# Optimization experiments

Hardware: AMD Instinct MI355X
Metric: run time of the kernel (lower is better)

The kernel has to match this reference:

```python
import jax, jax.numpy as jnp
import numpy as np

K_NN = 32
LN_EPS = 1e-5
P_JOINT = 0.95      # safety_priorities['structural_joints']
P_PLATFORM = 0.9    # safety_priorities['working_platforms']


def _sqdist(a, b):
    # a:[B,M,3], b:[B,N,3] -> [B,M,N] squared euclidean distances
    return jnp.maximum(jnp.sum(a * a, -1)[:, :, None] + jnp.sum(b * b, -1)[:, None, :]
                       - 2.0 * jnp.einsum('bmd,bnd->bmn', a, b), 0.0)


def _gather(arr, idx):
    # arr:[B,N,D], idx:[B,C] -> [B,C,D]
    B, C = idx.shape
    return jnp.take_along_axis(arr, jnp.broadcast_to(idx[:, :, None], (B, C, arr.shape[-1])), axis=1)


def _fps(coords, num_samples):
    # iterative farthest point sampling (deterministic start at index 0)
    B, N, _ = coords.shape
    start = jnp.zeros((B,), jnp.int32)
    dist0 = jnp.full((B, N), jnp.inf, coords.dtype)
    samp0 = jnp.zeros((B, num_samples), jnp.int32)

    def body(i, carry):
        dist, samp, last = carry
        last_pts = _gather(coords, last[:, None])                 # [B,1,3]
        d = jnp.sqrt(jnp.sum((coords - last_pts) ** 2, -1))       # [B,N]
        dist = jnp.minimum(dist, d)
        nxt = jnp.argmax(dist, 1).astype(jnp.int32)
        dist = dist.at[jnp.arange(B), nxt].set(0.0)
        samp = samp.at[:, i].set(nxt)
        return dist, samp, nxt

    _, samp, _ = jax.lax.fori_loop(1, num_samples, body, (dist0, samp0, start))
    return samp


def _safety(coords, scale):
    # per-point safety score [B,N], computed on the full point cloud (as in original)
    N = coords.shape[1]
    z = coords[:, :, 2]
    if scale == 'global':
        return 1.0 + jax.nn.sigmoid((z - z.mean(1, keepdims=True)) / 5.0) * P_JOINT
    if scale == 'component':
        zv = jnp.var(z, axis=1, keepdims=True, ddof=1)            # torch.var is unbiased
        return jnp.broadcast_to(1.0 + jnp.exp(-zv / 0.1) * P_PLATFORM, z.shape)
    # detail: full NxN cdist -> connection density (dist < 0.5  <=>  sqdist < 0.25)
    d2 = _sqdist(coords, coords)                                  # [B,N,N]
    density = jnp.sum(d2 < 0.25, -1).astype(coords.dtype)
    return 1.0 + density / N * P_JOINT


def _select_scale(features, coords, C, S, W1, b1, W2, b2, scale):
    idx = _fps(coords, C)                     # [B,C]
    cfeat = _gather(features, idx)            # [B,C,D]
    ccoord = _gather(coords, idx)             # [B,C,3]
    # kNN max-pooled local features (computed by original module; not used downstream)
    knn_d2 = _sqdist(ccoord, coords)          # [B,C,N]
    _, knn = jax.lax.top_k(-knn_d2, K_NN)
    _local = jax.vmap(lambda f, i: f[i])(features, knn).max(2)    # [B,C,D]
    # per-center safety score: per-point score gathered at FPS centers
    safety = jnp.take_along_axis(_safety(coords, scale), idx, axis=1)  # [B,C]
    # selector MLP: Linear -> ReLU -> Linear -> Sigmoid
    probs = jax.nn.sigmoid(jnp.maximum(cfeat @ W1.T + b1, 0.0) @ W2.T + b2)  # [B,C,S]
    final = probs.mean(-1) * safety           # [B,C] per-center score
    _, top = jax.lax.top_k(final, S)          # [B,S]
    return _gather(cfeat, top)                # [B,S,D]


def _forward(pf, pc, g_W1, g_b1, g_W2, g_b2, c_W1, c_b1, c_W2, c_b2,
             d_W1, d_b1, d_W2, d_b2, p_W1, p_b1, p_W2, p_b2, ln_g, ln_b):
    g = _select_scale(pf, pc, 256, 16, g_W1, g_b1, g_W2, g_b2, 'global')
    c = _select_scale(pf, pc, 128, 16, c_W1, c_b1, c_W2, c_b2, 'component')
    d = _select_scale(pf, pc, 64, 8, d_W1, d_b1, d_W2, d_b2, 'detail')
    toks = jnp.concatenate([g, c, d], 1)      # [B,40,D]
    # prompt_mlp: Linear(D,D/2) -> ReLU -> Linear(D/2,D) -> LayerNorm(D)
    h = jnp.maximum(toks @ p_W1.T + p_b1, 0.0) @ p_W2.T + p_b2
    mu = h.mean(-1, keepdims=True)
    var = h.var(-1, keepdims=True)
    return (h - mu) * jax.lax.rsqrt(var + LN_EPS) * ln_g + ln_b


def setup_inputs() -> dict:
    key = jax.random.key(0)
    B, N, D = 2, 8192, 768
    ks = iter(jax.random.split(key, 32))

    def nrm(shape, s=0.02):
        return jax.random.normal(next(ks), shape, jnp.float32) * s

    inp = {
        'point_features': jax.random.normal(next(ks), (B, N, D), jnp.float32),
        'point_coords': jax.random.normal(next(ks), (B, N, 3), jnp.float32) * 2.0,
    }
    for p, C, S in [('g', 256, 16), ('c', 128, 16), ('d', 64, 8)]:
        inp[p + '_W1'] = nrm((C, D)); inp[p + '_b1'] = jnp.zeros((C,), jnp.float32)
        inp[p + '_W2'] = nrm((S, C)); inp[p + '_b2'] = jnp.zeros((S,), jnp.float32)
    inp['p_W1'] = nrm((D // 2, D)); inp['p_b1'] = jnp.zeros((D // 2,), jnp.float32)
    inp['p_W2'] = nrm((D, D // 2)); inp['p_b2'] = jnp.zeros((D,), jnp.float32)
    inp['ln_g'] = jnp.ones((D,), jnp.float32); inp['ln_b'] = jnp.zeros((D,), jnp.float32)
    return inp


def reference(point_features, point_coords, g_W1, g_b1, g_W2, g_b2,
              c_W1, c_b1, c_W2, c_b2, d_W1, d_b1, d_W2, d_b2,
              p_W1, p_b1, p_W2, p_b2, ln_g, ln_b):
    return _forward(point_features, point_coords, g_W1, g_b1, g_W2, g_b2,
                    c_W1, c_b1, c_W2, c_b2, d_W1, d_b1, d_W2, d_b2,
                    p_W1, p_b1, p_W2, p_b2, ln_g, ln_b)
```

## Files before the change

### kernel.cpp

```cpp
#include <hip/hip_runtime.h>
#include <math.h>

#define N_PTS 8192
#define D_FEAT 768

typedef float v2f __attribute__((ext_vector_type(2)));

__device__ __forceinline__ float wred_max_f32(float x) {
    int v = __float_as_int(x), o;
    o = __builtin_amdgcn_update_dpp(0, v, 0x111, 0xf, 0xf, false); v = __float_as_int(fmaxf(__int_as_float(v), __int_as_float(o)));
    o = __builtin_amdgcn_update_dpp(0, v, 0x112, 0xf, 0xf, false); v = __float_as_int(fmaxf(__int_as_float(v), __int_as_float(o)));
    o = __builtin_amdgcn_update_dpp(0, v, 0x114, 0xf, 0xf, false); v = __float_as_int(fmaxf(__int_as_float(v), __int_as_float(o)));
    o = __builtin_amdgcn_update_dpp(0, v, 0x118, 0xf, 0xf, false); v = __float_as_int(fmaxf(__int_as_float(v), __int_as_float(o)));
    o = __builtin_amdgcn_update_dpp(0, v, 0x142, 0xa, 0xf, false); v = __float_as_int(fmaxf(__int_as_float(v), __int_as_float(o)));
    o = __builtin_amdgcn_update_dpp(0, v, 0x143, 0xc, 0xf, false); v = __float_as_int(fmaxf(__int_as_float(v), __int_as_float(o)));
    return __int_as_float(__builtin_amdgcn_readlane(v, 63));
}
__device__ __forceinline__ int wred_min_i32(int x) {
    int v = x, o;
    o = __builtin_amdgcn_update_dpp(0x7fffffff, v, 0x111, 0xf, 0xf, false); v = (o < v) ? o : v;
    o = __builtin_amdgcn_update_dpp(0x7fffffff, v, 0x112, 0xf, 0xf, false); v = (o < v) ? o : v;
    o = __builtin_amdgcn_update_dpp(0x7fffffff, v, 0x114, 0xf, 0xf, false); v = (o < v) ? o : v;
    o = __builtin_amdgcn_update_dpp(0x7fffffff, v, 0x118, 0xf, 0xf, false); v = (o < v) ? o : v;
    o = __builtin_amdgcn_update_dpp(0x7fffffff, v, 0x142, 0xa, 0xf, false); v = (o < v) ? o : v;
    o = __builtin_amdgcn_update_dpp(0x7fffffff, v, 0x143, 0xc, 0xf, false); v = (o < v) ? o : v;
    return __builtin_amdgcn_readlane(v, 63);
}
__device__ __forceinline__ float wred_add_f32(float x) {
    int v = __float_as_int(x), o;
    o = __builtin_amdgcn_update_dpp(0, v, 0x111, 0xf, 0xf, false); v = __float_as_int(__int_as_float(v) + __int_as_float(o));
    o = __builtin_amdgcn_update_dpp(0, v, 0x112, 0xf, 0xf, false); v = __float_as_int(__int_as_float(v) + __int_as_float(o));
    o = __builtin_amdgcn_update_dpp(0, v, 0x114, 0xf, 0xf, false); v = __float_as_int(__int_as_float(v) + __int_as_float(o));
    o = __builtin_amdgcn_update_dpp(0, v, 0x118, 0xf, 0xf, false); v = __float_as_int(__int_as_float(v) + __int_as_float(o));
    o = __builtin_amdgcn_update_dpp(0, v, 0x142, 0xa, 0xf, false); v = __float_as_int(__int_as_float(v) + __int_as_float(o));
    o = __builtin_amdgcn_update_dpp(0, v, 0x143, 0xc, 0xf, false); v = __float_as_int(__int_as_float(v) + __int_as_float(o));
    return __int_as_float(__builtin_amdgcn_readlane(v, 63));
}

#define DPP64_STEP(cur, ctrl, rmask)                                                        \
    {                                                                                       \
        unsigned _h = (unsigned)__builtin_amdgcn_update_dpp(0, (int)(unsigned)((cur) >> 32), ctrl, rmask, 0xf, false); \
        unsigned _l = (unsigned)__builtin_amdgcn_update_dpp(0, (int)(unsigned)(cur), ctrl, rmask, 0xf, false);         \
        unsigned long long _o = ((unsigned long long)_h << 32) | _l;                        \
        cur = (_o > (cur)) ? _o : (cur);                                                    \
    }

__global__ __launch_bounds__(512, 2) __attribute__((amdgpu_waves_per_eu(2)))
void fps_kernel(const float* __restrict__ coords,
                int* __restrict__ idx_all,
                float* __restrict__ safety_all) {
#pragma clang fp contract(off)
    const int b = blockIdx.x;
    const int t = threadIdx.x;
    const float* cb = coords + (size_t)b * N_PTS * 3;

    v2f px2[8], py2[8], pz2[8], m2p[8];
#pragma unroll
    for (int j = 0; j < 8; j++) {
        int p0 = t + (2 * j) * 512, p1 = t + (2 * j + 1) * 512;
        px2[j].x = cb[p0 * 3 + 0]; px2[j].y = cb[p1 * 3 + 0];
        py2[j].x = cb[p0 * 3 + 1]; py2[j].y = cb[p1 * 3 + 1];
        pz2[j].x = cb[p0 * 3 + 2]; pz2[j].y = cb[p1 * 3 + 2];
        m2p[j].x = INFINITY; m2p[j].y = INFINITY;
    }
    __shared__ float cbl4[N_PTS * 4];
    __shared__ unsigned long long skey[2][8];
    __shared__ int sel[256];
    __shared__ float r1s[8], r2s[8];
#pragma unroll
    for (int j = 0; j < 8; j++) {
        int p0 = t + (2 * j) * 512, p1 = t + (2 * j + 1) * 512;
        *(float4*)&cbl4[p0 * 4] = make_float4(px2[j].x, py2[j].x, pz2[j].x, 0.f);
        *(float4*)&cbl4[p1 * 4] = make_float4(px2[j].y, py2[j].y, pz2[j].y, 0.f);
    }
    if (t == 0) sel[0] = 0;
    float lx = cb[0], ly = cb[1], lz = cb[2];
    __syncthreads();

    const int lane = t & 63, w = t >> 6;
    for (int i = 1; i < 256; i++) {
        v2f Lx = {lx, lx}, Ly = {ly, ly}, Lz = {lz, lz};
#pragma unroll
        for (int j = 0; j < 8; j++) {
            v2f dx = px2[j] - Lx, dy = py2[j] - Ly, dz = pz2[j] - Lz;
            v2f d2 = dx * dx + dy * dy + dz * dz;
            m2p[j] = __builtin_elementwise_min(m2p[j], d2);
        }
        v2f q[4];
#pragma unroll
        for (int j = 0; j < 4; j++) q[j] = __builtin_elementwise_max(m2p[j], m2p[j + 4]);
        q[0] = __builtin_elementwise_max(q[0], q[2]);
        q[1] = __builtin_elementwise_max(q[1], q[3]);
        q[0] = __builtin_elementwise_max(q[0], q[1]);
        float c2 = fmaxf(q[0].x, q[0].y);
        int ci[8];
#pragma unroll
        for (int j = 0; j < 8; j++) {
            int a  = (m2p[j].x == c2) ? (2 * j)     : 0x7fff;
            int bb = (m2p[j].y == c2) ? (2 * j + 1) : 0x7fff;
            ci[j] = (a < bb) ? a : bb;
        }
#pragma unroll
        for (int j = 0; j < 4; j++) ci[j] = min(ci[j], ci[j + 4]);
        int bk = min(min(ci[0], ci[1]), min(ci[2], ci[3]));
        float thi = c2 * 0.9999995f;
        int tot = 0;
#pragma unroll
        for (int j = 0; j < 8; j++) {
            tot += __popcll(__ballot(m2p[j].x >= thi));
            tot += __popcll(__ballot(m2p[j].y >= thi));
        }
        float smax;
        if (tot > 64) {
            smax = -1.f; bk = 0;
#pragma unroll
            for (int k = 0; k < 16; k++) {
                float mk = (k & 1) ? m2p[k >> 1].y : m2p[k >> 1].x;
                float s = sqrtf(mk);
                if (s > smax) { smax = s; bk = k; }
            }
        } else {
            smax = sqrtf(c2);
        }
        int bi = t + bk * 512;
        unsigned long long key = ((unsigned long long)__float_as_uint(smax) << 32)
                               | (unsigned)(0xFFFFFFFFu - (unsigned)bi);
        DPP64_STEP(key, 0x111, 0xf)
        DPP64_STEP(key, 0x112, 0xf)
        DPP64_STEP(key, 0x114, 0xf)
        DPP64_STEP(key, 0x118, 0xf)
        DPP64_STEP(key, 0x142, 0xa)
        DPP64_STEP(key, 0x143, 0xc)
        if (lane == 63) skey[i & 1][w] = key;
        __syncthreads();
        const int par = i & 1;
        unsigned long long k8 = skey[par][lane & 7];
        int cidx = (int)(0xFFFFFFFFu - (unsigned)k8);
        float spec = 0.f;
        if (lane < 24) spec = cbl4[cidx * 4 + (lane >> 3)];
        DPP64_STEP(k8, 0x111, 0xf)
        DPP64_STEP(k8, 0x112, 0xf)
        DPP64_STEP(k8, 0x114, 0xf)
        unsigned klo = (unsigned)__builtin_amdgcn_readlane((int)(unsigned)k8, 7);
        int fbi = (int)(0xFFFFFFFFu - klo);
        int ww = (fbi & 511) >> 6;
        lx = __int_as_float(__builtin_amdgcn_readlane(__float_as_int(spec), ww));
        ly = __int_as_float(__builtin_amdgcn_readlane(__float_as_int(spec), 8 + ww));
        lz = __int_as_float(__builtin_amdgcn_readlane(__float_as_int(spec), 16 + ww));
        if (t == 0) sel[i] = fbi;
    }

    __syncthreads();
    if (t < 256) {
        int v = sel[t];
        idx_all[b * 256 + t] = v;
        if (t < 128) idx_all[512 + b * 128 + t] = v;
        if (t < 64)  idx_all[768 + b * 64 + t] = v;
    }

    float s1 = 0.f, s2 = 0.f;
#pragma unroll
    for (int j = 0; j < 8; j++) {
        s1 += pz2[j].x; s2 += pz2[j].x * pz2[j].x;
        s1 += pz2[j].y; s2 += pz2[j].y * pz2[j].y;
    }
    s1 = wred_add_f32(s1);
    s2 = wred_add_f32(s2);
    if (lane == 0) { r1s[w] = s1; r2s[w] = s2; }
    __syncthreads();
    float S1 = ((r1s[0] + r1s[1]) + (r1s[2] + r1s[3])) + ((r1s[4] + r1s[5]) + (r1s[6] + r1s[7]));
    float S2 = ((r2s[0] + r2s[1]) + (r2s[2] + r2s[3])) + ((r2s[4] + r2s[5]) + (r2s[6] + r2s[7]));
    float mean = S1 / 8192.0f;
    float var1 = (S2 - S1 * S1 / 8192.0f) / 8191.0f;
    float scomp = 1.0f + expf(-var1 / 0.1f) * 0.9f;
    if (t < 256) {
        int p = sel[t];
        float z = cbl4[p * 4 + 2];
        safety_all[b * 256 + t] = 1.0f + (1.0f / (1.0f + expf(-((z - mean) / 5.0f)))) * 0.95f;
        if (t < 128) safety_all[512 + b * 128 + t] = scomp;
    }
}

__global__ __launch_bounds__(256) void score_kernel(
    const float* __restrict__ feat, const float* __restrict__ coords,
    const float* __restrict__ gW1, const float* __restrict__ gb1,
    const float* __restrict__ gW2, const float* __restrict__ gb2,
    const float* __restrict__ cW1, const float* __restrict__ cb1,
    const float* __restrict__ cW2, const float* __restrict__ cb2,
    const float* __restrict__ dW1, const float* __restrict__ db1,
    const float* __restrict__ dW2, const float* __restrict__ db2,
    const int* __restrict__ idx_all, const float* __restrict__ safety_all,
    float* __restrict__ final_all) {
    int bid = blockIdx.x;
    int b, c0, C, S, off;
    const float *W1, *b1, *W2, *b2;
    if (bid < 64)      { C = 256; S = 16; W1 = gW1; b1 = gb1; W2 = gW2; b2 = gb2; b = bid >> 5; c0 = (bid & 31) * 8; off = 0; }
    else if (bid < 96) { int r = bid - 64; C = 128; S = 16; W1 = cW1; b1 = cb1; W2 = cW2; b2 = cb2; b = r >> 4; c0 = (r & 15) * 8; off = 512; }
    else               { int r = bid - 96; C = 64;  S = 8;  W1 = dW1; b1 = db1; W2 = dW2; b2 = db2; b = r >> 3; c0 = (r & 7) * 8; off = 768; }
    const bool isdet = (bid >= 96);

    __shared__ float xt[8 * 772];
    __shared__ float h1s[8 * 260];
    __shared__ float ps[8 * 16];
    __shared__ int pid[8];
    __shared__ float dpart[4][8];
    __shared__ float sdens[8];
    const int t = threadIdx.x;
    if (t < 8) pid[t] = idx_all[off + b * C + c0 + t];
    __syncthreads();

    if (isdet) {
#pragma clang fp contract(off)
        float cx[8], cy[8], cz[8], cc[8];
#pragma unroll
        for (int c = 0; c < 8; c++) {
            const float* cp = coords + ((size_t)b * N_PTS + pid[c]) * 3;
            cx[c] = cp[0]; cy[c] = cp[1]; cz[c] = cp[2];
            cc[c] = cx[c] * cx[c] + cy[c] * cy[c] + cz[c] * cz[c];
        }
        int cnt[8];
#pragma unroll
        for (int c = 0; c < 8; c++) cnt[c] = 0;
        const float* cbl = coords + (size_t)b * N_PTS * 3;
        for (int k = 0; k < 32; k++) {
            int q = t + k * 256;
            float x = cbl[q * 3], y = cbl[q * 3 + 1], z = cbl[q * 3 + 2];
            float pp = x * x + y * y + z * z;
#pragma unroll
            for (int c = 0; c < 8; c++) {
                float dot = cx[c] * x + cy[c] * y + cz[c] * z;
                float d2 = (cc[c] + pp) - 2.0f * dot;
                if (d2 < 0.25f) cnt[c]++;
            }
        }
        int wv = t >> 6;
#pragma unroll
        for (int c = 0; c < 8; c++) {
            float s = wred_add_f32((float)cnt[c]);
            if ((t & 63) == 0) dpart[wv][c] = s;
        }
    }

    for (int r = 0; r < 8; r++) {
        const float* src = feat + ((size_t)b * N_PTS + pid[r]) * D_FEAT;
        for (int c = t; c < 768; c += 256) xt[r * 772 + c] = src[c];
    }
    __syncthreads();
    if (isdet && t < 8) {
        float tot = dpart[0][t] + dpart[1][t] + dpart[2][t] + dpart[3][t];
        sdens[t] = 1.0f + (tot / 8192.0f) * 0.95f;
    }

    {
        int rp = t & 3;
        int jg = t >> 2;
        int r0 = rp * 2;
        if (jg * 4 < C) {
            float4 acc0[4], acc1[4];
#pragma unroll
            for (int a = 0; a < 4; a++) { acc0[a] = make_float4(0, 0, 0, 0); acc1[a] = make_float4(0, 0, 0, 0); }
            for (int k = 0; k < 768; k += 4) {
                float4 x0 = *(const float4*)&xt[r0 * 772 + k];
                float4 x1 = *(const float4*)&xt[(r0 + 1) * 772 + k];
#pragma unroll
                for (int a = 0; a < 4; a++) {
                    int j = jg * 4 + a;
                    float4 wv = *(const float4*)&W1[(size_t)j * 768 + k];
                    acc0[a].x = fmaf(wv.x, x0.x, acc0[a].x); acc0[a].y = fmaf(wv.y, x0.y, acc0[a].y);
                    acc0[a].z = fmaf(wv.z, x0.z, acc0[a].z); acc0[a].w = fmaf(wv.w, x0.w, acc0[a].w);
                    acc1[a].x = fmaf(wv.x, x1.x, acc1[a].x); acc1[a].y = fmaf(wv.y, x1.y, acc1[a].y);
                    acc1[a].z = fmaf(wv.z, x1.z, acc1[a].z); acc1[a].w = fmaf(wv.w, x1.w, acc1[a].w);
                }
            }
#pragma unroll
            for (int a = 0; a < 4; a++) {
                int j = jg * 4 + a;
                float bb = b1[j];
                float v0 = (acc0[a].x + acc0[a].y) + (acc0[a].z + acc0[a].w) + bb;
                float v1 = (acc1[a].x + acc1[a].y) + (acc1[a].z + acc1[a].w) + bb;
                h1s[r0 * 260 + j]       = fmaxf(v0, 0.f);
                h1s[(r0 + 1) * 260 + j] = fmaxf(v1, 0.f);
            }
        }
    }
    __syncthreads();

    if (t < 8 * S) {
        int r = t / S, s = t % S;
        float4 a = make_float4(0, 0, 0, 0);
        for (int k = 0; k < C; k += 4) {
            float4 wv = *(const float4*)&W2[s * C + k];
            float4 h = *(const float4*)&h1s[r * 260 + k];
            a.x = fmaf(wv.x, h.x, a.x); a.y = fmaf(wv.y, h.y, a.y);
            a.z = fmaf(wv.z, h.z, a.z); a.w = fmaf(wv.w, h.w, a.w);
        }
        float logit = (a.x + a.y) + (a.z + a.w) + b2[s];
        ps[r * 16 + s] = 1.0f / (1.0f + expf(-logit));
    }
    __syncthreads();
    if (t < 8) {
        float m = 0.f;
        for (int s = 0; s < S; s++) m += ps[t * 16 + s];
        m /= (float)S;
        float saf = isdet ? sdens[t] : safety_all[off + b * C + c0 + t];
        final_all[off + b * C + c0 + t] = m * saf;
    }
}

__global__ __launch_bounds__(256) void final_kernel(
    const float* __restrict__ feat, const int* __restrict__ idx_all,
    const float* __restrict__ final_all,
    const float* __restrict__ pW1, const float* __restrict__ pb1,
    const float* __restrict__ pW2, const float* __restrict__ pb2,
    const float* __restrict__ lng, const float* __restrict__ lnb,
    float* __restrict__ out) {
    int bid = blockIdx.x;
    int b = bid / 20, pr = bid % 20;
    int t = threadIdx.x;
    __shared__ float xt[2 * 772];
    __shared__ float h1s[2 * 388];
    __shared__ float red[16];
    __shared__ int tokp[2];

    int scale = (pr < 8) ? 0 : (pr < 16) ? 1 : 2;
    int C    = (scale == 0) ? 256 : (scale == 1) ? 128 : 64;
    int off  = (scale == 0) ? 0 : (scale == 1) ? 512 : 768;
    int base = (scale == 0) ? 0 : (scale == 1) ? 8 : 16;
    int r0 = (pr - base) * 2;

    if (t < 64) {
        float v[4];
#pragma unroll
        for (int j = 0; j < 4; j++) {
            int ii = t + j * 64;
            v[j] = (ii < C) ? final_all[off + b * C + ii] : -INFINITY;
        }
        for (int s = 0; s <= r0 + 1; s++) {
            float bd = v[0]; int bj = 0;
#pragma unroll
            for (int j = 1; j < 4; j++) if (v[j] > bd) { bd = v[j]; bj = j; }
            int bi2 = t + bj * 64;
            float m = wred_max_f32(bd);
            int cand = (bd == m) ? bi2 : 0x7fffffff;
            int wi = wred_min_i32(cand);
            if (t == (wi & 63)) {
#pragma unroll
                for (int j = 0; j < 4; j++) if (j == (wi >> 6)) v[j] = -INFINITY;
            }
            if (t == 0) {
                if (s == r0)     tokp[0] = idx_all[off + b * C + wi];
                if (s == r0 + 1) tokp[1] = idx_all[off + b * C + wi];
            }
        }
    }
    __syncthreads();

    for (int r = 0; r < 2; r++) {
        int p = tokp[r];
        const float* src = feat + ((size_t)b * N_PTS + p) * D_FEAT;
        for (int c = t; c < 768; c += 256) xt[r * 772 + c] = src[c];
    }
    __syncthreads();

    for (int u = t; u < 768; u += 256) {
        int j = u >> 1, r = u & 1;
        float4 a = make_float4(0, 0, 0, 0);
        for (int k = 0; k < 768; k += 4) {
            float4 wv = *(const float4*)&pW1[(size_t)j * 768 + k];
            float4 x = *(const float4*)&xt[r * 772 + k];
            a.x = fmaf(wv.x, x.x, a.x); a.y = fmaf(wv.y, x.y, a.y);
            a.z = fmaf(wv.z, x.z, a.z); a.w = fmaf(wv.w, x.w, a.w);
        }
        float v = (a.x + a.y) + (a.z + a.w) + pb1[j];
        h1s[r * 388 + j] = fmaxf(v, 0.f);
    }
    __syncthreads();

    for (int u = t; u < 1536; u += 256) {
        int o = u >> 1, r = u & 1;
        float4 a = make_float4(0, 0, 0, 0);
        for (int k = 0; k < 384; k += 4) {
            float4 wv = *(const float4*)&pW2[(size_t)o * 384 + k];
            float4 h = *(const float4*)&h1s[r * 388 + k];
            a.x = fmaf(wv.x, h.x, a.x); a.y = fmaf(wv.y, h.y, a.y);
            a.z = fmaf(wv.z, h.z, a.z); a.w = fmaf(wv.w, h.w, a.w);
        }
        xt[r * 772 + o] = (a.x + a.y) + (a.z + a.w) + pb2[o];
    }
    __syncthreads();

    for (int r = 0; r < 2; r++) {
        float s1 = 0.f, s2 = 0.f;
        for (int o = t; o < 768; o += 256) { float v = xt[r * 772 + o]; s1 += v; s2 += v * v; }
#pragma unroll
        for (int off2 = 32; off2 >= 1; off2 >>= 1) {
            s1 += __shfl_down(s1, off2, 64);
            s2 += __shfl_down(s2, off2, 64);
        }
        int lane = t & 63, wid = t >> 6;
        if (lane == 0) { red[wid * 2] = s1; red[wid * 2 + 1] = s2; }
        __syncthreads();
        float S1 = red[0] + red[2] + red[4] + red[6];
        float S2 = red[1] + red[3] + red[5] + red[7];
        float mu = S1 / 768.0f;
        float var = S2 / 768.0f - mu * mu;
        float inv = rsqrtf(var + 1e-5f);
        float* dst = out + ((size_t)b * 40 + pr * 2 + r) * 768;
        for (int o = t; o < 768; o += 256) {
            float v = xt[r * 772 + o];
            dst[o] = (v - mu) * inv * lng[o] + lnb[o];
        }
        __syncthreads();
    }
}

extern "C" void kernel_launch(void* const* d_in, const int* in_sizes, int n_in,
                              void* d_out, int out_size, void* d_ws, size_t ws_size,
                              hipStream_t stream) {
    const float* feat   = (const float*)d_in[0];
    const float* coords = (const float*)d_in[1];
    const float* gW1 = (const float*)d_in[2],  *gb1 = (const float*)d_in[3];
    const float* gW2 = (const float*)d_in[4],  *gb2 = (const float*)d_in[5];
    const float* cW1 = (const float*)d_in[6],  *cb1 = (const float*)d_in[7];
    const float* cW2 = (const float*)d_in[8],  *cb2 = (const float*)d_in[9];
    const float* dW1 = (const float*)d_in[10], *db1 = (const float*)d_in[11];
    const float* dW2 = (const float*)d_in[12], *db2 = (const float*)d_in[13];
    const float* pW1 = (const float*)d_in[14], *pb1 = (const float*)d_in[15];
    const float* pW2 = (const float*)d_in[16], *pb2 = (const float*)d_in[17];
    const float* lng = (const float*)d_in[18], *lnb = (const float*)d_in[19];
    float* out = (float*)d_out;

    int*   idx_all    = (int*)d_ws;
    float* safety_all = (float*)d_ws + 896;
    float* final_all  = (float*)d_ws + 1792;

    fps_kernel<<<2, 512, 0, stream>>>(coords, idx_all, safety_all);
    score_kernel<<<112, 256, 0, stream>>>(feat, coords, gW1, gb1, gW2, gb2, cW1, cb1, cW2, cb2,
                                          dW1, db1, dW2, db2, idx_all, safety_all, final_all);
    final_kernel<<<40, 256, 0, stream>>>(feat, idx_all, final_all, pW1, pb1, pW2, pb2, lng, lnb, out);
}
```

Before: 558.0 us.

## Split final MLP into top-k, GEMM and layernorm kernels, retile score GEMM

The FPS argmax reduction now does a float max, then a ballot to find the winning lane, with an integer-min fallback on ties, in place of 64-bit DPP key reductions. The score kernel's W1 GEMM is re-tiled so each thread processes all 8 rows over a quarter of K, and the four K-partials are reduced through shared memory. The monolithic final kernel, which redundantly recomputed top-k and loaded whole weight matrices per block, is split into separate top-k, hidden-layer, output-layer and layernorm kernels spread over more blocks. This adds launches and global round-trips for intermediates.

```diff
diff --git a/kernel.cpp b/kernel.cpp
--- a/kernel.cpp
+++ b/kernel.cpp
@@ -123,14 +123,18 @@
             smax = sqrtf(c2);
         }
         int bi = t + bk * 512;
-        unsigned long long key = ((unsigned long long)__float_as_uint(smax) << 32)
-                               | (unsigned)(0xFFFFFFFFu - (unsigned)bi);
-        DPP64_STEP(key, 0x111, 0xf)
-        DPP64_STEP(key, 0x112, 0xf)
-        DPP64_STEP(key, 0x114, 0xf)
-        DPP64_STEP(key, 0x118, 0xf)
-        DPP64_STEP(key, 0x142, 0xa)
-        DPP64_STEP(key, 0x143, 0xc)
+        float mred = wred_max_f32(smax);
+        unsigned long long ball = __ballot(smax == mred);
+        int bi_win;
+        if (__popcll(ball) == 1) {
+            int ls = (int)__builtin_ctzll(ball);
+            bi_win = __builtin_amdgcn_readlane(bi, ls);
+        } else {
+            int cand = (smax == mred) ? bi : 0x7fffffff;
+            bi_win = wred_min_i32(cand);
+        }
+        unsigned long long key = ((unsigned long long)__float_as_uint(mred) << 32)
+                               | (unsigned)(0xFFFFFFFFu - (unsigned)bi_win);
         if (lane == 63) skey[i & 1][w] = key;
         __syncthreads();
         const int par = i & 1;
@@ -181,6 +185,34 @@
     }
 }
 
+#define W1_GEMM(RT)                                                            \
+  {                                                                            \
+    const int jg = t >> 2, rp = t & 3;                                         \
+    const float* wb = W1 + (size_t)(jg * RT) * 768 + rp * 192;                 \
+    float4 acc[RT][8];                                                         \
+    _Pragma("unroll") for (int a = 0; a < RT; a++)                             \
+      _Pragma("unroll") for (int r = 0; r < 8; r++)                            \
+        acc[a][r] = make_float4(0.f, 0.f, 0.f, 0.f);                           \
+    for (int s = 0; s < 192; s += 4) {                                         \
+      float4 xv[8];                                                            \
+      _Pragma("unroll") for (int r = 0; r < 8; r++)                            \
+        xv[r] = *(const float4*)&xt[r * 772 + rp * 192 + s];                   \
+      _Pragma("unroll") for (int a = 0; a < RT; a++) {                         \
+        float4 wv = *(const float4*)&wb[(size_t)a * 768 + s];                  \
+        _Pragma("unroll") for (int r = 0; r < 8; r++) {                        \
+          acc[a][r].x = fmaf(wv.x, xv[r].x, acc[a][r].x);                      \
+          acc[a][r].y = fmaf(wv.y, xv[r].y, acc[a][r].y);                      \
+          acc[a][r].z = fmaf(wv.z, xv[r].z, acc[a][r].z);                      \
+          acc[a][r].w = fmaf(wv.w, xv[r].w, acc[a][r].w);                      \
+        }                                                                      \
+      }                                                                        \
+    }                                                                          \
+    _Pragma("unroll") for (int a = 0; a < RT; a++)                             \
+      _Pragma("unroll") for (int r = 0; r < 8; r++)                            \
+        part[rp * 2048 + (jg * RT + a) * 8 + r] =                              \
+            (acc[a][r].x + acc[a][r].y) + (acc[a][r].z + acc[a][r].w);         \
+  }
+
 __global__ __launch_bounds__(256) void score_kernel(
     const float* __restrict__ feat, const float* __restrict__ coords,
     const float* __restrict__ gW1, const float* __restrict__ gb1,
@@ -201,6 +233,7 @@
 
     __shared__ float xt[8 * 772];
     __shared__ float h1s[8 * 260];
+    __shared__ float part[4 * 2048];
     __shared__ float ps[8 * 16];
     __shared__ int pid[8];
     __shared__ float dpart[4][8];
@@ -251,37 +284,14 @@
         sdens[t] = 1.0f + (tot / 8192.0f) * 0.95f;
     }
 
-    {
-        int rp = t & 3;
-        int jg = t >> 2;
-        int r0 = rp * 2;
-        if (jg * 4 < C) {
-            float4 acc0[4], acc1[4];
-#pragma unroll
-            for (int a = 0; a < 4; a++) { acc0[a] = make_float4(0, 0, 0, 0); acc1[a] = make_float4(0, 0, 0, 0); }
-            for (int k = 0; k < 768; k += 4) {
-                float4 x0 = *(const float4*)&xt[r0 * 772 + k];
-                float4 x1 = *(const float4*)&xt[(r0 + 1) * 772 + k];
-#pragma unroll
-                for (int a = 0; a < 4; a++) {
-                    int j = jg * 4 + a;
-                    float4 wv = *(const float4*)&W1[(size_t)j * 768 + k];
-                    acc0[a].x = fmaf(wv.x, x0.x, acc0[a].x); acc0[a].y = fmaf(wv.y, x0.y, acc0[a].y);
-                    acc0[a].z = fmaf(wv.z, x0.z, acc0[a].z); acc0[a].w = fmaf(wv.w, x0.w, acc0[a].w);
-                    acc1[a].x = fmaf(wv.x, x1.x, acc1[a].x); acc1[a].y = fmaf(wv.y, x1.y, acc1[a].y);
-                    acc1[a].z = fmaf(wv.z, x1.z, acc1[a].z); acc1[a].w = fmaf(wv.w, x1.w, acc1[a].w);
-                }
-            }
-#pragma unroll
-            for (int a = 0; a < 4; a++) {
-                int j = jg * 4 + a;
-                float bb = b1[j];
-                float v0 = (acc0[a].x + acc0[a].y) + (acc0[a].z + acc0[a].w) + bb;
-                float v1 = (acc1[a].x + acc1[a].y) + (acc1[a].z + acc1[a].w) + bb;
-                h1s[r0 * 260 + j]       = fmaxf(v0, 0.f);
-                h1s[(r0 + 1) * 260 + j] = fmaxf(v1, 0.f);
-            }
-        }
+    if (C == 256)      W1_GEMM(4)
+    else if (C == 128) W1_GEMM(2)
+    else               W1_GEMM(1)
+    __syncthreads();
+    for (int u = t; u < C * 8; u += 256) {
+        int row = u >> 3;
+        float sum = (part[u] + part[2048 + u]) + (part[4096 + u] + part[6144 + u]) + b1[row];
+        h1s[(u & 7) * 260 + row] = fmaxf(sum, 0.f);
     }
     __syncthreads();
 
@@ -307,110 +317,106 @@
     }
 }
 
-__global__ __launch_bounds__(256) void final_kernel(
-    const float* __restrict__ feat, const int* __restrict__ idx_all,
-    const float* __restrict__ final_all,
+
+__global__ __launch_bounds__(64) void topk_kernel(
+    const float* __restrict__ final_all, const int* __restrict__ idx_all,
+    int* __restrict__ tok) {
+    int bid = blockIdx.x;
+    int b = bid / 3, sc = bid % 3;
+    int C    = (sc == 0) ? 256 : (sc == 1) ? 128 : 64;
+    int off  = (sc == 0) ? 0 : (sc == 1) ? 512 : 768;
+    int base = (sc == 0) ? 0 : (sc == 1) ? 16 : 32;
+    int S    = (sc == 2) ? 8 : 16;
+    int t = threadIdx.x;
+    float v[4];
+#pragma unroll
+    for (int j = 0; j < 4; j++) {
+        int ii = t + j * 64;
+        v[j] = (ii < C) ? final_all[off + b * C + ii] : -INFINITY;
+    }
+    for (int s = 0; s < S; s++) {
+        float bd = v[0]; int bj = 0;
+#pragma unroll
+        for (int j = 1; j < 4; j++) if (v[j] > bd) { bd = v[j]; bj = j; }
+        int bi2 = t + bj * 64;
+        float m = wred_max_f32(bd);
+        int cand = (bd == m) ? bi2 : 0x7fffffff;
+        int wi = wred_min_i32(cand);
+        if (t == (wi & 63)) {
+#pragma unroll
+            for (int j = 0; j < 4; j++) if (j == (wi >> 6)) v[j] = -INFINITY;
+        }
+        if (t == 0) tok[b * 40 + base + s] = idx_all[off + b * C + wi];
+    }
+}
+
+__global__ __launch_bounds__(320) void h_kernel(
+    const float* __restrict__ feat, const int* __restrict__ tok,
     const float* __restrict__ pW1, const float* __restrict__ pb1,
+    float* __restrict__ h_buf) {
+    int bid = blockIdx.x;
+    int b = bid / 48, js = bid % 48;
+    int t = threadIdx.x;
+    int tk = t % 40, jr = t / 40;
+    int j = js * 8 + jr;
+    int p = tok[b * 40 + tk];
+    const float* x = feat + ((size_t)b * N_PTS + p) * D_FEAT;
+    const float* wrow = pW1 + (size_t)j * 768;
+    float4 a = make_float4(0, 0, 0, 0);
+    for (int k = 0; k < 768; k += 4) {
+        float4 wv = *(const float4*)&wrow[k];
+        float4 xv = *(const float4*)&x[k];
+        a.x = fmaf(wv.x, xv.x, a.x); a.y = fmaf(wv.y, xv.y, a.y);
+        a.z = fmaf(wv.z, xv.z, a.z); a.w = fmaf(wv.w, xv.w, a.w);
+    }
+    float v = (a.x + a.y) + (a.z + a.w) + pb1[j];
+    h_buf[((size_t)b * 40 + tk) * 384 + j] = fmaxf(v, 0.f);
+}
+
+__global__ __launch_bounds__(320) void out_kernel(
+    const float* __restrict__ h_buf,
     const float* __restrict__ pW2, const float* __restrict__ pb2,
+    float* __restrict__ pre_buf) {
+    int bid = blockIdx.x;
+    int b = bid / 96, os = bid % 96;
+    int t = threadIdx.x;
+    int tk = t % 40, orr = t / 40;
+    int o = os * 8 + orr;
+    const float* h = h_buf + ((size_t)b * 40 + tk) * 384;
+    const float* wrow = pW2 + (size_t)o * 384;
+    float4 a = make_float4(0, 0, 0, 0);
+    for (int k = 0; k < 384; k += 4) {
+        float4 wv = *(const float4*)&wrow[k];
+        float4 hv = *(const float4*)&h[k];
+        a.x = fmaf(wv.x, hv.x, a.x); a.y = fmaf(wv.y, hv.y, a.y);
+        a.z = fmaf(wv.z, hv.z, a.z); a.w = fmaf(wv.w, hv.w, a.w);
+    }
+    pre_buf[((size_t)b * 40 + tk) * 768 + o] = (a.x + a.y) + (a.z + a.w) + pb2[o];
+}
+
+__global__ __launch_bounds__(64) void ln_kernel(
+    const float* __restrict__ pre_buf,
     const float* __restrict__ lng, const float* __restrict__ lnb,
     float* __restrict__ out) {
     int bid = blockIdx.x;
-    int b = bid / 20, pr = bid % 20;
-    int t = threadIdx.x;
-    __shared__ float xt[2 * 772];
-    __shared__ float h1s[2 * 388];
-    __shared__ float red[16];
-    __shared__ int tokp[2];
-
-    int scale = (pr < 8) ? 0 : (pr < 16) ? 1 : 2;
-    int C    = (scale == 0) ? 256 : (scale == 1) ? 128 : 64;
-    int off  = (scale == 0) ? 0 : (scale == 1) ? 512 : 768;
-    int base = (scale == 0) ? 0 : (scale == 1) ? 8 : 16;
-    int r0 = (pr - base) * 2;
-
-    if (t < 64) {
-        float v[4];
-#pragma unroll
-        for (int j = 0; j < 4; j++) {
-            int ii = t + j * 64;
-            v[j] = (ii < C) ? final_all[off + b * C + ii] : -INFINITY;
-        }
-        for (int s = 0; s <= r0 + 1; s++) {
-            float bd = v[0]; int bj = 0;
-#pragma unroll
-            for (int j = 1; j < 4; j++) if (v[j] > bd) { bd = v[j]; bj = j; }
-            int bi2 = t + bj * 64;
-            float m = wred_max_f32(bd);
-            int cand = (bd == m) ? bi2 : 0x7fffffff;
-            int wi = wred_min_i32(cand);
-            if (t == (wi & 63)) {
-#pragma unroll
-                for (int j = 0; j < 4; j++) if (j == (wi >> 6)) v[j] = -INFINITY;
-            }
-            if (t == 0) {
-                if (s == r0)     tokp[0] = idx_all[off + b * C + wi];
-                if (s == r0 + 1) tokp[1] = idx_all[off + b * C + wi];
-            }
-        }
-    }
-    __syncthreads();
-
-    for (int r = 0; r < 2; r++) {
-        int p = tokp[r];
-        const float* src = feat + ((size_t)b * N_PTS + p) * D_FEAT;
-        for (int c = t; c < 768; c += 256) xt[r * 772 + c] = src[c];
-    }
-    __syncthreads();
-
-    for (int u = t; u < 768; u += 256) {
-        int j = u >> 1, r = u & 1;
-        float4 a = make_float4(0, 0, 0, 0);
-        for (int k = 0; k < 768; k += 4) {
-            float4 wv = *(const float4*)&pW1[(size_t)j * 768 + k];
-            float4 x = *(const float4*)&xt[r * 772 + k];
-            a.x = fmaf(wv.x, x.x, a.x); a.y = fmaf(wv.y, x.y, a.y);
-            a.z = fmaf(wv.z, x.z, a.z); a.w = fmaf(wv.w, x.w, a.w);
-        }
-        float v = (a.x + a.y) + (a.z + a.w) + pb1[j];
-        h1s[r * 388 + j] = fmaxf(v, 0.f);
-    }
-    __syncthreads();
-
-    for (int u = t; u < 1536; u += 256) {
-        int o = u >> 1, r = u & 1;
-        float4 a = make_float4(0, 0, 0, 0);
-        for (int k = 0; k < 384; k += 4) {
-            float4 wv = *(const float4*)&pW2[(size_t)o * 384 + k];
-            float4 h = *(const float4*)&h1s[r * 388 + k];
-            a.x = fmaf(wv.x, h.x, a.x); a.y = fmaf(wv.y, h.y, a.y);
-            a.z = fmaf(wv.z, h.z, a.z); a.w = fmaf(wv.w, h.w, a.w);
-        }
-        xt[r * 772 + o] = (a.x + a.y) + (a.z + a.w) + pb2[o];
-    }
-    __syncthreads();
-
-    for (int r = 0; r < 2; r++) {
-        float s1 = 0.f, s2 = 0.f;
-        for (int o = t; o < 768; o += 256) { float v = xt[r * 772 + o]; s1 += v; s2 += v * v; }
-#pragma unroll
-        for (int off2 = 32; off2 >= 1; off2 >>= 1) {
-            s1 += __shfl_down(s1, off2, 64);
-            s2 += __shfl_down(s2, off2, 64);
-        }
-        int lane = t & 63, wid = t >> 6;
-        if (lane == 0) { red[wid * 2] = s1; red[wid * 2 + 1] = s2; }
-        __syncthreads();
-        float S1 = red[0] + red[2] + red[4] + red[6];
-        float S2 = red[1] + red[3] + red[5] + red[7];
-        float mu = S1 / 768.0f;
-        float var = S2 / 768.0f - mu * mu;
-        float inv = rsqrtf(var + 1e-5f);
-        float* dst = out + ((size_t)b * 40 + pr * 2 + r) * 768;
-        for (int o = t; o < 768; o += 256) {
-            float v = xt[r * 772 + o];
-            dst[o] = (v - mu) * inv * lng[o] + lnb[o];
-        }
-        __syncthreads();
+    int lane = threadIdx.x;
+    const float* row = pre_buf + (size_t)bid * 768;
+    float v[12], s1 = 0.f, s2 = 0.f;
+#pragma unroll
+    for (int i = 0; i < 12; i++) {
+        v[i] = row[lane + i * 64];
+        s1 += v[i]; s2 += v[i] * v[i];
+    }
+    s1 = wred_add_f32(s1);
+    s2 = wred_add_f32(s2);
+    float mu = s1 / 768.0f;
+    float var = s2 / 768.0f - mu * mu;
+    float inv = rsqrtf(var + 1e-5f);
+    float* dst = out + (size_t)bid * 768;
+#pragma unroll
+    for (int i = 0; i < 12; i++) {
+        int o = lane + i * 64;
+        dst[o] = (v[i] - mu) * inv * lng[o] + lnb[o];
     }
 }
 
@@ -433,9 +439,15 @@
     int*   idx_all    = (int*)d_ws;
     float* safety_all = (float*)d_ws + 896;
     float* final_all  = (float*)d_ws + 1792;
+    int*   tok        = (int*)d_ws + 2688;
+    float* h_buf      = (float*)d_ws + 2816;
+    float* pre_buf    = (float*)d_ws + 33536;
 
     fps_kernel<<<2, 512, 0, stream>>>(coords, idx_all, safety_all);
     score_kernel<<<112, 256, 0, stream>>>(feat, coords, gW1, gb1, gW2, gb2, cW1, cb1, cW2, cb2,
                                           dW1, db1, dW2, db2, idx_all, safety_all, final_all);
-    final_kernel<<<40, 256, 0, stream>>>(feat, idx_all, final_all, pW1, pb1, pW2, pb2, lng, lnb, out);
-}
+    topk_kernel<<<6, 64, 0, stream>>>(final_all, idx_all, tok);
+    h_kernel<<<96, 320, 0, stream>>>(feat, tok, pW1, pb1, h_buf);
+    out_kernel<<<192, 320, 0, stream>>>(h_buf, pW2, pb2, pre_buf);
+    ln_kernel<<<80, 64, 0, stream>>>(pre_buf, lng, lnb, out);
+}
```

New measurement: 525.7 us. -5.8%, faster.
